# Performance work log

Measured on AMD Instinct MI355X. Metric: run time of the kernel, lower is better.

Reference implementation:

```python
import jax, jax.numpy as jnp
import numpy as np

N = 1_600_000  # number of rows/messages
D = 128        # feature dim
V_NODES = 50_000


def setup_inputs() -> dict:
    key = jax.random.key(0)
    k1, k2 = jax.random.split(key)
    H = jax.random.normal(k1, (N, D), dtype=jnp.float32)
    X_node = jax.random.randint(k2, (N,), 0, V_NODES, dtype=jnp.int32)
    return {"H": H, "X_node": X_node, "V": V_NODES}


def reference(H, X_node, V):
    # Original builds a dense [V, N] one-hot mask (mask[v, n] = 1 iff X_node[n] == v)
    # and computes mm(mask, H). Mathematically this is exactly a segment sum of the
    # rows of H grouped by X_node into V buckets, which we compute directly.
    return jax.ops.segment_sum(H, X_node, num_segments=V)
```

## Files before the change

kernel.cpp:

```cpp
#include <hip/hip_runtime.h>


#define D 128
#define BLOCK 256
#define CAP 128

typedef float f2 __attribute__((ext_vector_type(2)));

__global__ void scatter_kernel(const int* __restrict__ idx, int* __restrict__ count,
                               int* __restrict__ order, int* __restrict__ ovf_meta,
                               int* __restrict__ ovf, int n) {
    int i = blockIdx.x * blockDim.x + threadIdx.x;
    int stride = gridDim.x * blockDim.x;
    for (; i < n; i += stride) {
        const int v = idx[i];
        const int p = atomicAdd(&count[v], 1);
        if (p < CAP) {
            order[((unsigned)v << 7) | p] = i;
        } else {
            const int q = atomicAdd(ovf_meta, 1);
            ovf[q] = i;
        }
    }
}

__global__ void __launch_bounds__(BLOCK) reduce_kernel(const f2* __restrict__ H2,
                                                       const int* __restrict__ count,
                                                       const int* __restrict__ order,
                                                       f2* __restrict__ out, int V) {
    const int gid  = blockIdx.x * blockDim.x + threadIdx.x;
    const int wave = gid >> 6;
    if (wave >= V) return;
    const int lane = gid & 63;

    int cnt = count[wave];
    if (cnt > CAP) cnt = CAP;
    const int*  base  = order + ((size_t)wave << 7);
    const int4* base4 = (const int4*)base;

    f2 acc = {0.f, 0.f};
    int g = 0;
    for (; g + 8 <= cnt; g += 8) {
        const int4 i0 = base4[(g >> 2) + 0];
        const int4 i1 = base4[(g >> 2) + 1];
        const f2 a0 = __builtin_nontemporal_load(H2 + (((unsigned)i0.x << 6) | lane));
        const f2 a1 = __builtin_nontemporal_load(H2 + (((unsigned)i0.y << 6) | lane));
        const f2 a2 = __builtin_nontemporal_load(H2 + (((unsigned)i0.z << 6) | lane));
        const f2 a3 = __builtin_nontemporal_load(H2 + (((unsigned)i0.w << 6) | lane));
        const f2 a4 = __builtin_nontemporal_load(H2 + (((unsigned)i1.x << 6) | lane));
        const f2 a5 = __builtin_nontemporal_load(H2 + (((unsigned)i1.y << 6) | lane));
        const f2 a6 = __builtin_nontemporal_load(H2 + (((unsigned)i1.z << 6) | lane));
        const f2 a7 = __builtin_nontemporal_load(H2 + (((unsigned)i1.w << 6) | lane));
        acc += ((a0 + a1) + (a2 + a3)) + ((a4 + a5) + (a6 + a7));
    }
    if (g < cnt) {
#pragma unroll
        for (int k = 0; k < 7; ++k) {
            const int j  = g + k;
            const int jj = (j < cnt) ? j : (cnt - 1);
            const int n  = base[jj];
            const f2 a = __builtin_nontemporal_load(H2 + (((unsigned)n << 6) | lane));
            const float m = (j < cnt) ? 1.f : 0.f;
            acc.x = fmaf(m, a.x, acc.x);
            acc.y = fmaf(m, a.y, acc.y);
        }
    }
    __builtin_nontemporal_store(acc, out + (((unsigned)wave << 6) | lane));
}

__global__ void ovf_fix_kernel(const f2* __restrict__ H2, const int* __restrict__ idx,
                               const int* __restrict__ ovf_meta, const int* __restrict__ ovf,
                               float* __restrict__ out) {
    const int novf = *ovf_meta;
    if (novf <= 0) return;
    const int gid  = blockIdx.x * blockDim.x + threadIdx.x;
    const int wave = gid >> 6;
    const int lane = gid & 63;
    const int nwaves = (gridDim.x * blockDim.x) >> 6;
    for (int o = wave; o < novf; o += nwaves) {
        const int row = ovf[o];
        const int v   = idx[row];
        const f2 a = H2[(((unsigned)row) << 6) | lane];
        atomicAdd(&out[((unsigned)v << 7) | ((unsigned)lane << 1)],       a.x);
        atomicAdd(&out[(((unsigned)v << 7) | ((unsigned)lane << 1)) + 1], a.y);
    }
}

extern "C" void kernel_launch(void* const* d_in, const int* in_sizes, int n_in,
                              void* d_out, int out_size, void* d_ws, size_t ws_size,
                              hipStream_t stream) {
    const float* H      = (const float*)d_in[0];
    const int*   X_node = (const int*)d_in[1];
    const int N = in_sizes[1];
    const int V = out_size / D;
    float* out = (float*)d_out;

    int* count    = (int*)d_ws;
    int* ovf_meta = count + V;
    int* ovf      = ovf_meta + 1;
    int* order    = ovf + N;

    hipMemsetAsync(count, 0, ((size_t)V + 1) * sizeof(int), stream);

    scatter_kernel<<<2048, BLOCK, 0, stream>>>(X_node, count, order, ovf_meta, ovf, N);

    reduce_kernel<<<((size_t)V * 64 + BLOCK - 1) / BLOCK, BLOCK, 0, stream>>>(
        (const f2*)H, count, order, (f2*)out, V);

    ovf_fix_kernel<<<16, BLOCK, 0, stream>>>((const f2*)H, X_node, ovf_meta, ovf, out);
}
```

Baseline: 314.9 us.

## Window H rows into cache-sized chunks with cooperative prefetch before gather-reduce

Splits the N rows into 16 windows and buckets indices per (window, node) cell, so the reduce kernel processes one window of H at a time, with each wave owning 13 nodes. While gathering from the current window, all waves cooperatively stream the next window of H with coalesced loads, aiming to warm L2/MALL so the random row gathers hit cache instead of HBM. This adds redundant streaming reads of H, 16x larger count/order workspace, more register pressure from 13 accumulators, and only about 3.8k waves, which lowers parallelism. Per-cell capacity drops to 16, so more rows may spill to the atomic overflow path.

```diff
diff --git a/kernel.cpp b/kernel.cpp
--- a/kernel.cpp
+++ b/kernel.cpp
@@ -3,69 +3,93 @@
 
 #define D 128
 #define BLOCK 256
-#define CAP 128
+#define W 16
+#define CAPW 16
+#define BPW 13
 
 typedef float f2 __attribute__((ext_vector_type(2)));
+typedef float f4 __attribute__((ext_vector_type(4)));
 
-__global__ void scatter_kernel(const int* __restrict__ idx, int* __restrict__ count,
+__global__ void scatter_kernel(const int* __restrict__ idx, int* __restrict__ cnt,
                                int* __restrict__ order, int* __restrict__ ovf_meta,
-                               int* __restrict__ ovf, int n) {
+                               int* __restrict__ ovf, int n, int rpw, int V) {
     int i = blockIdx.x * blockDim.x + threadIdx.x;
     int stride = gridDim.x * blockDim.x;
     for (; i < n; i += stride) {
         const int v = idx[i];
-        const int p = atomicAdd(&count[v], 1);
-        if (p < CAP) {
-            order[((unsigned)v << 7) | p] = i;
-        } else {
-            const int q = atomicAdd(ovf_meta, 1);
-            ovf[q] = i;
-        }
+        const int w = i / rpw;
+        const int cell = w * V + v;
+        const int p = atomicAdd(&cnt[cell], 1);
+        if (p < CAPW) order[(size_t)cell * CAPW + p] = i;
+        else { int q = atomicAdd(ovf_meta, 1); ovf[q] = i; }
     }
 }
 
-__global__ void __launch_bounds__(BLOCK) reduce_kernel(const f2* __restrict__ H2,
-                                                       const int* __restrict__ count,
-                                                       const int* __restrict__ order,
-                                                       f2* __restrict__ out, int V) {
+__global__ void __launch_bounds__(BLOCK, 4) reduce_kernel(
+        const f2* __restrict__ H2, const f4* __restrict__ H4,
+        const int* __restrict__ cnt, const int* __restrict__ order,
+        f2* __restrict__ out, int V, int N, int rpw, int nwaves) {
     const int gid  = blockIdx.x * blockDim.x + threadIdx.x;
-    const int wave = gid >> 6;
-    if (wave >= V) return;
+    const int wv   = gid >> 6;
     const int lane = gid & 63;
+    const int b0   = wv * BPW;
 
-    int cnt = count[wave];
-    if (cnt > CAP) cnt = CAP;
-    const int*  base  = order + ((size_t)wave << 7);
-    const int4* base4 = (const int4*)base;
+    f2 acc[BPW];
+#pragma unroll
+    for (int b = 0; b < BPW; ++b) acc[b] = (f2){0.f, 0.f};
 
-    f2 acc = {0.f, 0.f};
-    int g = 0;
-    for (; g + 8 <= cnt; g += 8) {
-        const int4 i0 = base4[(g >> 2) + 0];
-        const int4 i1 = base4[(g >> 2) + 1];
-        const f2 a0 = __builtin_nontemporal_load(H2 + (((unsigned)i0.x << 6) | lane));
-        const f2 a1 = __builtin_nontemporal_load(H2 + (((unsigned)i0.y << 6) | lane));
-        const f2 a2 = __builtin_nontemporal_load(H2 + (((unsigned)i0.z << 6) | lane));
-        const f2 a3 = __builtin_nontemporal_load(H2 + (((unsigned)i0.w << 6) | lane));
-        const f2 a4 = __builtin_nontemporal_load(H2 + (((unsigned)i1.x << 6) | lane));
-        const f2 a5 = __builtin_nontemporal_load(H2 + (((unsigned)i1.y << 6) | lane));
-        const f2 a6 = __builtin_nontemporal_load(H2 + (((unsigned)i1.z << 6) | lane));
-        const f2 a7 = __builtin_nontemporal_load(H2 + (((unsigned)i1.w << 6) | lane));
-        acc += ((a0 + a1) + (a2 + a3)) + ((a4 + a5) + (a6 + a7));
-    }
-    if (g < cnt) {
-#pragma unroll
-        for (int k = 0; k < 7; ++k) {
-            const int j  = g + k;
-            const int jj = (j < cnt) ? j : (cnt - 1);
-            const int n  = base[jj];
-            const f2 a = __builtin_nontemporal_load(H2 + (((unsigned)n << 6) | lane));
-            const float m = (j < cnt) ? 1.f : 0.f;
-            acc.x = fmaf(m, a.x, acc.x);
-            acc.y = fmaf(m, a.y, acc.y);
+    const long h4n = (long)N * 32;
+    const long w4  = (long)rpw * 32;
+    const int pfl = (int)((w4 + (long)nwaves * 64 - 1) / ((long)nwaves * 64));
+
+    float sink = 0.f;
+
+    {
+        const long we = (w4 < h4n) ? w4 : h4n;
+        long p = (long)wv * (pfl * 64) + lane;
+        for (int k = 0; k < pfl; ++k, p += 64) {
+            if (p < we) { const f4 t = H4[p]; sink += t.x; }
         }
     }
-    __builtin_nontemporal_store(acc, out + (((unsigned)wave << 6) | lane));
+
+#pragma unroll 1
+    for (int w = 0; w < W; ++w) {
+        if (w + 1 < W) {
+            const long wb = (long)(w + 1) * w4;
+            long we = wb + w4; if (we > h4n) we = h4n;
+            long p = wb + (long)wv * (pfl * 64) + lane;
+            for (int k = 0; k < pfl; ++k, p += 64) {
+                if (p < we) { const f4 t = H4[p]; sink += t.x; }
+            }
+        }
+#pragma unroll
+        for (int b = 0; b < BPW; ++b) {
+            const int v = b0 + b;
+            if (v < V) {
+                const int cell = w * V + v;
+                int c = cnt[cell]; c = (c > CAPW) ? CAPW : c;
+                const int* op = order + (size_t)cell * CAPW;
+                for (int g = 0; g < c; g += 2) {
+                    const int2 iv = *(const int2*)(op + g);
+                    const int  j1 = (g + 1 < c) ? iv.y : iv.x;
+                    const f2 a0 = H2[(size_t)(unsigned)iv.x * 64 + lane];
+                    const f2 a1 = H2[(size_t)(unsigned)j1   * 64 + lane];
+                    const float m1 = (g + 1 < c) ? 1.f : 0.f;
+                    acc[b].x += a0.x;
+                    acc[b].y += a0.y;
+                    acc[b].x = fmaf(m1, a1.x, acc[b].x);
+                    acc[b].y = fmaf(m1, a1.y, acc[b].y);
+                }
+            }
+        }
+    }
+    asm volatile("" :: "v"(sink));
+
+#pragma unroll
+    for (int b = 0; b < BPW; ++b) {
+        const int v = b0 + b;
+        if (v < V) out[(size_t)v * 64 + lane] = acc[b];
+    }
 }
 
 __global__ void ovf_fix_kernel(const f2* __restrict__ H2, const int* __restrict__ idx,
@@ -80,9 +104,9 @@
     for (int o = wave; o < novf; o += nwaves) {
         const int row = ovf[o];
         const int v   = idx[row];
-        const f2 a = H2[(((unsigned)row) << 6) | lane];
-        atomicAdd(&out[((unsigned)v << 7) | ((unsigned)lane << 1)],       a.x);
-        atomicAdd(&out[(((unsigned)v << 7) | ((unsigned)lane << 1)) + 1], a.y);
+        const f2 a = H2[(size_t)(unsigned)row * 64 + lane];
+        atomicAdd(&out[((size_t)v << 7) | ((unsigned)lane << 1)],       a.x);
+        atomicAdd(&out[(((size_t)v << 7) | ((unsigned)lane << 1)) + 1], a.y);
     }
 }
 
@@ -95,17 +119,22 @@
     const int V = out_size / D;
     float* out = (float*)d_out;
 
-    int* count    = (int*)d_ws;
-    int* ovf_meta = count + V;
+    const int rpw = (N + W - 1) / W;
+
+    int* cnt      = (int*)d_ws;
+    int* ovf_meta = cnt + (size_t)V * W;
     int* ovf      = ovf_meta + 1;
     int* order    = ovf + N;
 
-    hipMemsetAsync(count, 0, ((size_t)V + 1) * sizeof(int), stream);
+    hipMemsetAsync(cnt, 0, ((size_t)V * W + 1) * sizeof(int), stream);
 
-    scatter_kernel<<<2048, BLOCK, 0, stream>>>(X_node, count, order, ovf_meta, ovf, N);
+    scatter_kernel<<<2048, BLOCK, 0, stream>>>(X_node, cnt, order, ovf_meta, ovf,
+                                               N, rpw, V);
 
-    reduce_kernel<<<((size_t)V * 64 + BLOCK - 1) / BLOCK, BLOCK, 0, stream>>>(
-        (const f2*)H, count, order, (f2*)out, V);
+    const int nwaves = (V + BPW - 1) / BPW;
+    const int blocks = (nwaves + 3) / 4;
+    reduce_kernel<<<blocks, BLOCK, 0, stream>>>(
+        (const f2*)H, (const f4*)H, cnt, order, (f2*)out, V, N, rpw, blocks * 4);
 
     ovf_fix_kernel<<<16, BLOCK, 0, stream>>>((const f2*)H, X_node, ovf_meta, ovf, out);
 }
```

Measured after the change: 613.4 us. 94.8% more time.
